# Kernel optimization log

Hardware: AMD Instinct MI355X
Metric: run time of the kernel (lower is better)

The kernel has to match this reference:

```python
import jax, jax.numpy as jnp
import numpy as np

SEQ, BATCH = 256, 8
N_NODES = SEQ * BATCH
VOCAB, D_MODEL, H, D_K, D_FF, N_LAYERS, MAX_POS = 259, 256, 8, 32, 1024, 2, 128


def setup_inputs() -> dict:
    key = jax.random.key(0)
    ks = jax.random.split(key, 16)
    # structured causal edge list per sequence (dst attends to src <= dst, incl. self)
    tri_dst, tri_src = np.tril_indices(SEQ)
    offs = (np.arange(BATCH) * SEQ)[:, None]
    edge_src = jnp.asarray((tri_src[None, :] + offs).ravel(), dtype=jnp.int64)
    edge_dst = jnp.asarray((tri_dst[None, :] + offs).ravel(), dtype=jnp.int64)
    positions = jnp.tile(jnp.arange(SEQ, dtype=jnp.int64), BATCH)
    tokens = jax.random.randint(ks[0], (N_NODES,), 0, VOCAB, dtype=jnp.int64)
    s = 0.02
    p = lambda k, shp: jax.random.normal(k, shp, dtype=jnp.float32) * s
    return {
        "tokens": tokens, "positions": positions,
        "edge_src": edge_src, "edge_dst": edge_dst,
        "coord_emb": p(ks[1], (3, D_MODEL)),
        "pos_emb": p(ks[2], (MAX_POS, D_MODEL)),
        "value_emb": p(ks[3], (VOCAB, D_MODEL)),
        "ln1_scale": jnp.ones((N_LAYERS, D_MODEL)), "ln1_bias": jnp.zeros((N_LAYERS, D_MODEL)),
        "Wqkv": p(ks[4], (N_LAYERS, D_MODEL, 3 * D_MODEL)),
        "Wo": p(ks[5], (N_LAYERS, D_MODEL, D_MODEL)),
        "ln2_scale": jnp.ones((N_LAYERS, D_MODEL)), "ln2_bias": jnp.zeros((N_LAYERS, D_MODEL)),
        "W1": p(ks[6], (N_LAYERS, D_MODEL, D_FF)), "b1": jnp.zeros((N_LAYERS, D_FF)),
        "W2": p(ks[7], (N_LAYERS, D_FF, D_MODEL)), "b2": jnp.zeros((N_LAYERS, D_MODEL)),
        "lnf_scale": jnp.ones((D_MODEL,)), "lnf_bias": jnp.zeros((D_MODEL,)),
        "Wg": p(ks[8], (D_MODEL, VOCAB)), "bg": jnp.zeros((VOCAB,)),
    }


def _ln(x, scale, bias, eps=1e-5):
    mu = jnp.mean(x, axis=-1, keepdims=True)
    var = jnp.var(x, axis=-1, keepdims=True)
    return (x - mu) * jax.lax.rsqrt(var + eps) * scale + bias


def _graph_attention(x, src, dst, Wqkv, Wo, ln_s, ln_b):
    n = x.shape[0]
    xn = _ln(x, ln_s, ln_b)
    qkv = (xn @ Wqkv).reshape(n, 3, H, D_K)
    q, k, v = qkv[:, 0], qkv[:, 1], qkv[:, 2]  # [n, H, D_K] each
    # u_dot_v('k','q','score') per edge, scaled
    score = jnp.einsum("ehd,ehd->eh", k[src], q[dst]) / jnp.sqrt(jnp.float32(D_K))
    # edge_softmax over incoming edges of each dst node
    smax = jax.ops.segment_max(score, dst, num_segments=n)      # [n, H]
    ex = jnp.exp(score - smax[dst])                              # [E, H]
    denom = jax.ops.segment_sum(ex, dst, num_segments=n)        # [n, H]
    alpha = ex / denom[dst]
    # u_mul_e('v','softmax_score') + sum reduce -> z on dst nodes
    z = jax.ops.segment_sum(alpha[:, :, None] * v[src], dst, num_segments=n)  # [n, H, D_K]
    return x + z.reshape(n, D_MODEL) @ Wo


def reference(tokens, positions, edge_src, edge_dst, coord_emb, pos_emb, value_emb,
              ln1_scale, ln1_bias, Wqkv, Wo, ln2_scale, ln2_bias, W1, b1, W2, b2,
              lnf_scale, lnf_bias, Wg, bg):
    x = coord_emb[positions % 3] + pos_emb[positions // 3] + value_emb[tokens]
    for i in range(Wqkv.shape[0]):
        x = _graph_attention(x, edge_src, edge_dst, Wqkv[i], Wo[i], ln1_scale[i], ln1_bias[i])
        h = _ln(x, ln2_scale[i], ln2_bias[i])
        x = x + jax.nn.relu(h @ W1[i] + b1[i]) @ W2[i] + b2[i]
    out = _ln(x, lnf_scale, lnf_bias) @ Wg + bg
    return jax.nn.log_softmax(out, axis=-1)
```

## Files before the change

kernel.cpp:

```cpp
#include <hip/hip_runtime.h>
#include <hip/hip_bf16.h>

typedef __hip_bfloat16 bf16;
typedef unsigned short ushort_t;
typedef unsigned int uint_t;
typedef __attribute__((ext_vector_type(8))) short short8;
typedef __attribute__((ext_vector_type(4))) float floatx4;

#define D_MODEL 256
#define SEQ     256
#define BATCH   8
#define NN      2048
#define NHEAD   8
#define DK      32
#define DFF     1024
#define VOCAB   259
#define NLAYER  2

#define WQKVT_OFF 0
#define WOT_OFF   393216
#define W1T_OFF   524288
#define W2T_OFF   1048576
#define WGT_OFF   1572864
#define WT_TOTAL  1639168
#define LNP_TOTAL 2560
#define BP_TOTAL  2819

__device__ __forceinline__ ushort_t f2bs(float f) {
    bf16 h = __float2bfloat16(f);
    ushort_t u; __builtin_memcpy(&u, &h, 2); return u;
}
template<bool BF>
__device__ __forceinline__ float ldw(const void* p, int i) {
    if (BF) return __bfloat162float(((const bf16*)p)[i]);
    return ((const float*)p)[i];
}
template<bool BF>
__device__ __forceinline__ ushort_t ldb(const void* p, size_t i) {
    if (BF) return ((const ushort_t*)p)[i];
    return f2bs(((const float*)p)[i]);
}
template<bool I64>
__device__ __forceinline__ int ldi(const void* p, int i) {
    if (I64) return (int)(((const long long*)p)[i]);
    return ((const int*)p)[i];
}
__device__ __forceinline__ float wred_sum(float v) {
    #pragma unroll
    for (int m = 32; m > 0; m >>= 1) v += __shfl_xor(v, m, 64);
    return v;
}
__device__ __forceinline__ float wred_max(float v) {
    #pragma unroll
    for (int m = 32; m > 0; m >>= 1) v = fmaxf(v, __shfl_xor(v, m, 64));
    return v;
}
__device__ __forceinline__ bool detBF(const void* ln1s) {
    return *(const uint_t*)ln1s == 0x3F803F80u;
}
__device__ __forceinline__ bool detI64(const void* pos) {
    const int* p32 = (const int*)pos;
    return p32[1] == 0 && p32[2] == 1;
}

template<bool BF>
__device__ void ttile(const void* src, size_t srcOff, int K, int N, int tk, int tn,
                      ushort_t* dst, ushort_t (*tile)[72]) {
    int t = threadIdx.x;
    if ((N & 63) == 0) {
        #pragma unroll
        for (int pass = 0; pass < 2; ++pass) {
            int e = pass * 256 + t;
            int kl = e >> 3, ng = e & 7;
            size_t sbase = srcOff + (size_t)(tk*64 + kl) * N + tn*64 + ng*8;
            ushort_t v[8];
            if (BF) {
                *reinterpret_cast<uint4*>(v) =
                    *reinterpret_cast<const uint4*>((const ushort_t*)src + sbase);
            } else {
                float4 a = *reinterpret_cast<const float4*>((const float*)src + sbase);
                float4 b = *reinterpret_cast<const float4*>((const float*)src + sbase + 4);
                v[0]=f2bs(a.x); v[1]=f2bs(a.y); v[2]=f2bs(a.z); v[3]=f2bs(a.w);
                v[4]=f2bs(b.x); v[5]=f2bs(b.y); v[6]=f2bs(b.z); v[7]=f2bs(b.w);
            }
            *reinterpret_cast<uint4*>(&tile[kl][ng*8]) = *reinterpret_cast<const uint4*>(v);
        }
        __syncthreads();
        #pragma unroll
        for (int pass = 0; pass < 2; ++pass) {
            int e = pass * 256 + t;
            int nl = e >> 3, kg = e & 7;
            int n = tn * 64 + nl;
            ushort_t v[8];
            #pragma unroll
            for (int j = 0; j < 8; ++j) v[j] = tile[kg*8 + j][nl];
            *reinterpret_cast<uint4*>(dst + (size_t)n * K + tk*64 + kg*8) =
                *reinterpret_cast<const uint4*>(v);
        }
    } else {
        #pragma unroll
        for (int pass = 0; pass < 16; ++pass) {
            int e = pass * 256 + t;
            int kl = e >> 6, nl = e & 63;
            int n = tn * 64 + nl;
            tile[kl][nl] = (n < N) ? ldb<BF>(src, srcOff + (size_t)(tk*64 + kl) * N + n)
                                   : (ushort_t)0;
        }
        __syncthreads();
        #pragma unroll
        for (int pass = 0; pass < 16; ++pass) {
            int e = pass * 256 + t;
            int nl = e >> 6, kl = e & 63;
            int n = tn * 64 + nl;
            if (n < N) dst[(size_t)n * K + tk*64 + kl] = tile[kl][nl];
        }
    }
}

template<bool BF, bool I64>
__device__ void embedln16(const void* tok, const void* pos,
        const void* ce, const void* pe, const void* ve,
        const void* ln1s, const void* ln1b, int rowBase,
        float* x, ushort_t* xn) {
    int lane = threadIdx.x & 63, wave = threadIdx.x >> 6;
    #pragma unroll
    for (int i = 0; i < 4; ++i) {
        int n = rowBase + wave * 4 + i;
        int p  = ldi<I64>(pos, n);
        int tk = ldi<I64>(tok, n);
        int c0 = lane * 4;
        float v[4];
        #pragma unroll
        for (int j = 0; j < 4; ++j)
            v[j] = ldw<BF>(ce, (p % 3) * 256 + c0 + j)
                 + ldw<BF>(pe, (p / 3) * 256 + c0 + j)
                 + ldw<BF>(ve, tk * 256 + c0 + j);
        float s  = wred_sum(v[0] + v[1] + v[2] + v[3]);
        float s2 = wred_sum(v[0]*v[0] + v[1]*v[1] + v[2]*v[2] + v[3]*v[3]);
        float mu = s * (1.f/256.f);
        float var = s2 * (1.f/256.f) - mu * mu;
        float rstd = rsqrtf(var + 1e-5f);
        *reinterpret_cast<float4*>(&x[(size_t)n*256 + c0]) =
            make_float4(v[0], v[1], v[2], v[3]);
        ushort4 o;
        o.x = f2bs((v[0]-mu)*rstd*ldw<BF>(ln1s, c0+0) + ldw<BF>(ln1b, c0+0));
        o.y = f2bs((v[1]-mu)*rstd*ldw<BF>(ln1s, c0+1) + ldw<BF>(ln1b, c0+1));
        o.z = f2bs((v[2]-mu)*rstd*ldw<BF>(ln1s, c0+2) + ldw<BF>(ln1b, c0+2));
        o.w = f2bs((v[3]-mu)*rstd*ldw<BF>(ln1s, c0+3) + ldw<BF>(ln1b, c0+3));
        *reinterpret_cast<ushort4*>(&xn[(size_t)n*256 + c0]) = o;
    }
}

template<bool BF, bool I64>
__device__ void prep_body(const void* tok, const void* pos,
        const void* ce, const void* pe, const void* ve,
        const void* Wqkv, const void* Wo, const void* W1, const void* W2, const void* Wg,
        const void* ln1s, const void* ln1b, const void* ln2s, const void* ln2b,
        const void* lnfs, const void* lnfb,
        const void* b1, const void* b2, const void* bg,
        ushort_t* WT, float* lnP, float* bP, float* x, ushort_t* xn,
        ushort_t (*tile)[72]) {
    int blk = blockIdx.x;
    if (blk < 404) {
        const void* src; int K, N, tk, tn; size_t dstOff, srcOff;
        if (blk < 96)       { int L = blk/48, lo = blk%48; src=Wqkv; K=256; N=768;
                              srcOff=(size_t)L*196608; dstOff=WQKVT_OFF+(size_t)L*196608;
                              tk=lo/12; tn=lo%12; }
        else if (blk < 128) { int b2=blk-96, L=b2/16, lo=b2%16; src=Wo; K=256; N=256;
                              srcOff=(size_t)L*65536; dstOff=WOT_OFF+(size_t)L*65536;
                              tk=lo/4; tn=lo%4; }
        else if (blk < 256) { int b2=blk-128, L=b2/64, lo=b2%64; src=W1; K=256; N=1024;
                              srcOff=(size_t)L*262144; dstOff=W1T_OFF+(size_t)L*262144;
                              tk=lo/16; tn=lo%16; }
        else if (blk < 384) { int b2=blk-256, L=b2/64, lo=b2%64; src=W2; K=1024; N=256;
                              srcOff=(size_t)L*262144; dstOff=W2T_OFF+(size_t)L*262144;
                              tk=lo/4; tn=lo%4; }
        else                { int lo=blk-384; src=Wg; K=256; N=259;
                              srcOff=0; dstOff=WGT_OFF; tk=lo/5; tn=lo%5; }
        ttile<BF>(src, srcOff, K, N, tk, tn, WT + dstOff, tile);
    } else if (blk < 426) {
        int gid = (blk - 404) * 256 + threadIdx.x;
        if (gid < LNP_TOTAL) {
            float v;
            if      (gid < 512)  v = ldw<BF>(ln1s, gid);
            else if (gid < 1024) v = ldw<BF>(ln1b, gid - 512);
            else if (gid < 1536) v = ldw<BF>(ln2s, gid - 1024);
            else if (gid < 2048) v = ldw<BF>(ln2b, gid - 1536);
            else if (gid < 2304) v = ldw<BF>(lnfs, gid - 2048);
            else                 v = ldw<BF>(lnfb, gid - 2304);
            lnP[gid] = v;
        } else if (gid < LNP_TOTAL + BP_TOTAL) {
            int g = gid - LNP_TOTAL;
            float v;
            if      (g < 2048) v = ldw<BF>(b1, g);
            else if (g < 2560) v = ldw<BF>(b2, g - 2048);
            else               v = ldw<BF>(bg, g - 2560);
            bP[g] = v;
        }
    } else {
        embedln16<BF, I64>(tok, pos, ce, pe, ve, ln1s, ln1b, (blk - 426) * 16, x, xn);
    }
}

__global__ void __launch_bounds__(256) prep_k(const void* tok, const void* pos,
        const void* ce, const void* pe, const void* ve,
        const void* Wqkv, const void* Wo, const void* W1, const void* W2, const void* Wg,
        const void* ln1s, const void* ln1b, const void* ln2s, const void* ln2b,
        const void* lnfs, const void* lnfb,
        const void* b1, const void* b2, const void* bg,
        ushort_t* WT, float* lnP, float* bP, float* x, ushort_t* xn) {
    __shared__ ushort_t tile[64][72];
    bool BF = detBF(ln1s), I64 = detI64(pos);
    if (BF) { if (I64) prep_body<true,true >(tok,pos,ce,pe,ve,Wqkv,Wo,W1,W2,Wg,ln1s,ln1b,ln2s,ln2b,lnfs,lnfb,b1,b2,bg,WT,lnP,bP,x,xn,tile);
              else     prep_body<true,false>(tok,pos,ce,pe,ve,Wqkv,Wo,W1,W2,Wg,ln1s,ln1b,ln2s,ln2b,lnfs,lnfb,b1,b2,bg,WT,lnP,bP,x,xn,tile); }
    else    { if (I64) prep_body<false,true >(tok,pos,ce,pe,ve,Wqkv,Wo,W1,W2,Wg,ln1s,ln1b,ln2s,ln2b,lnfs,lnfb,b1,b2,bg,WT,lnP,bP,x,xn,tile);
              else     prep_body<false,false>(tok,pos,ce,pe,ve,Wqkv,Wo,W1,W2,Wg,ln1s,ln1b,ln2s,ln2b,lnfs,lnfb,b1,b2,bg,WT,lnP,bP,x,xn,tile); }
}

union AttnSH {
    struct {
        ushort_t Ks[SEQ][40];
        ushort_t Qs[64][40];
    } a;
    ushort_t Ps[64][264];
};
__global__ void __launch_bounds__(256) attn_k(const ushort_t* __restrict__ qkvB,
                                              ushort_t* __restrict__ zB,
                                              float* __restrict__ yZ) {
    __shared__ AttnSH u;
    __shared__ ushort_t Vt[32][264];
    int t = threadIdx.x;
    {
        float4 z4 = make_float4(0.f, 0.f, 0.f, 0.f);
        float4* yp = reinterpret_cast<float4*>(yZ + (size_t)blockIdx.x * 2048);
        yp[t]       = z4;
        yp[t + 256] = z4;
    }
    int lane = t & 63, wave = t >> 6;
    int quad = lane >> 4, l16 = lane & 15;
    int tile = blockIdx.x & 3, bh = blockIdx.x >> 2;
    int b = bh >> 3, h = bh & 7;
    int base = b * SEQ;
    int dstBase = tile * 64;
    int tileEnd = (tile + 1) * 64;

    int nV = tileEnd * 4;
    for (int i = t; i < nV; i += 256) {
        int src = i >> 2, g = i & 3;
        const ushort_t* rp = qkvB + (size_t)(base + src) * 768 + h * 32 + g * 8;
        uint4 kv = *reinterpret_cast<const uint4*>(rp + 256);
        *reinterpret_cast<uint4*>(&u.a.Ks[src][g * 8]) = kv;
        uint4 vv = *reinterpret_cast<const uint4*>(rp + 512);
        const ushort_t* vs = (const ushort_t*)&vv;
        #pragma unroll
        for (int j = 0; j < 8; ++j) Vt[g * 8 + j][src] = vs[j];
    }
    {
        int r = t >> 2, g = t & 3;
        uint4 qv = *reinterpret_cast<const uint4*>(
            qkvB + (size_t)(base + dstBase + r) * 768 + h * 32 + g * 8);
        *reinterpret_cast<uint4*>(&u.a.Qs[r][g * 8]) = qv;
    }
    __syncthreads();

    const float scale = 0.17677669529663687f;
    int stLim = tile * 4 + wave;
    int stCnt = stLim + 1;
    short8 qf = *reinterpret_cast<const short8*>(&u.a.Qs[wave * 16 + l16][quad * 8]);
    floatx4 accs[16];
    #pragma unroll
    for (int st = 0; st < 16; ++st) {
        if (st <= stLim) {
            short8 kf = *reinterpret_cast<const short8*>(&u.a.Ks[st * 16 + l16][quad * 8]);
            accs[st] = __builtin_amdgcn_mfma_f32_16x16x32_bf16(qf, kf, (floatx4){0.f,0.f,0.f,0.f}, 0, 0, 0);
        }
    }
    float mrow[4] = {-3e38f, -3e38f, -3e38f, -3e38f};
    #pragma unroll
    for (int st = 0; st < 16; ++st) {
        if (st <= stLim) {
            int srcg = st * 16 + l16;
            #pragma unroll
            for (int r = 0; r < 4; ++r) {
                int dstg = dstBase + wave * 16 + quad * 4 + r;
                float sv = (srcg <= dstg) ? accs[st][r] * scale : -3e38f;
                accs[st][r] = sv;
                mrow[r] = fmaxf(mrow[r], sv);
            }
        }
    }
    #pragma unroll
    for (int mk = 1; mk < 16; mk <<= 1)
        #pragma unroll
        for (int r = 0; r < 4; ++r) mrow[r] = fmaxf(mrow[r], __shfl_xor(mrow[r], mk, 64));
    float lrow[4] = {0.f, 0.f, 0.f, 0.f};
    #pragma unroll
    for (int st = 0; st < 16; ++st) {
        if (st <= stLim) {
            #pragma unroll
            for (int r = 0; r < 4; ++r) {
                float p = __expf(accs[st][r] - mrow[r]);
                accs[st][r] = p;
                lrow[r] += p;
            }
        }
    }
    #pragma unroll
    for (int mk = 1; mk < 16; mk <<= 1)
        #pragma unroll
        for (int r = 0; r < 4; ++r) lrow[r] += __shfl_xor(lrow[r], mk, 64);
    __syncthreads();

    #pragma unroll
    for (int st = 0; st < 16; ++st) {
        if (st <= stLim) {
            #pragma unroll
            for (int r = 0; r < 4; ++r)
                u.Ps[wave * 16 + quad * 4 + r][st * 16 + l16] = f2bs(accs[st][r]);
        }
    }
    if (stCnt & 1) {
        #pragma unroll
        for (int r = 0; r < 4; ++r)
            u.Ps[wave * 16 + quad * 4 + r][stCnt * 16 + l16] = 0;
    }
    __syncthreads();

    int ktCnt = (stCnt + 1) >> 1;
    floatx4 acco[2];
    acco[0] = (floatx4){0.f,0.f,0.f,0.f};
    acco[1] = (floatx4){0.f,0.f,0.f,0.f};
    #pragma unroll
    for (int kt = 0; kt < 8; ++kt) {
        if (kt < ktCnt) {
            short8 pf = *reinterpret_cast<const short8*>(&u.Ps[wave * 16 + l16][kt * 32 + quad * 8]);
            #pragma unroll
            for (int dn = 0; dn < 2; ++dn) {
                short8 vf = *reinterpret_cast<const short8*>(&Vt[dn * 16 + l16][kt * 32 + quad * 8]);
                acco[dn] = __builtin_amdgcn_mfma_f32_16x16x32_bf16(pf, vf, acco[dn], 0, 0, 0);
            }
        }
    }
    #pragma unroll
    for (int dn = 0; dn < 2; ++dn)
        #pragma unroll
        for (int r = 0; r < 4; ++r)
            zB[(size_t)(base + dstBase + wave * 16 + quad * 4 + r) * 256
               + h * 32 + dn * 16 + l16] = f2bs(acco[dn][r] / lrow[r]);
}

__global__ void __launch_bounds__(256) gemm_k(const ushort_t* __restrict__ A, int K,
        const ushort_t* __restrict__ BT, const float* __restrict__ bias,
        ushort_t* __restrict__ C, int ldc, int relu) {
    int t = threadIdx.x;
    int lane = t & 63, wave = t >> 6;
    int quad = lane >> 4, l16 = lane & 15;
    int wm = (wave >> 1) * 32, wn = (wave & 1) * 32;
    int rowBase = blockIdx.x * 64, colBase = blockIdx.y * 64;
    floatx4 acc[2][2];
    #pragma unroll
    for (int a = 0; a < 2; ++a)
        #pragma unroll
        for (int b = 0; b < 2; ++b) acc[a][b] = (floatx4){0.f,0.f,0.f,0.f};
    const ushort_t* a0 = A + (size_t)(rowBase + wm + l16) * K + quad * 8;
    const ushort_t* a1 = a0 + (size_t)16 * K;
    const ushort_t* b0 = BT + (size_t)(colBase + wn + l16) * K + quad * 8;
    const ushort_t* b1 = b0 + (size_t)16 * K;
    #pragma unroll 8
    for (int k0 = 0; k0 < K; k0 += 32) {
        short8 af0 = *reinterpret_cast<const short8*>(a0 + k0);
        short8 af1 = *reinterpret_cast<const short8*>(a1 + k0);
        short8 bf0 = *reinterpret_cast<const short8*>(b0 + k0);
        short8 bf1 = *reinterpret_cast<const short8*>(b1 + k0);
        acc[0][0] = __builtin_amdgcn_mfma_f32_16x16x32_bf16(af0, bf0, acc[0][0], 0,0,0);
        acc[0][1] = __builtin_amdgcn_mfma_f32_16x16x32_bf16(af0, bf1, acc[0][1], 0,0,0);
        acc[1][0] = __builtin_amdgcn_mfma_f32_16x16x32_bf16(af1, bf0, acc[1][0], 0,0,0);
        acc[1][1] = __builtin_amdgcn_mfma_f32_16x16x32_bf16(af1, bf1, acc[1][1], 0,0,0);
    }
    #pragma unroll
    for (int nt = 0; nt < 2; ++nt) {
        int col = colBase + wn + nt*16 + l16;
        float bb = bias ? bias[col] : 0.f;
        #pragma unroll
        for (int mt = 0; mt < 2; ++mt)
            #pragma unroll
            for (int r = 0; r < 4; ++r) {
                int row = rowBase + wm + mt*16 + quad*4 + r;
                float v = acc[mt][nt][r] + bb;
                if (relu) v = fmaxf(v, 0.f);
                C[(size_t)row * ldc + col] = f2bs(v);
            }
    }
}

__global__ void __launch_bounds__(256) tail_k(
        const ushort_t* __restrict__ zB, const ushort_t* __restrict__ WoT,
        const float* __restrict__ xIn,
        const float* __restrict__ ls2, const float* __restrict__ lb2,
        const ushort_t* __restrict__ W1T, const float* __restrict__ b1P,
        const ushort_t* __restrict__ W2T, const float* __restrict__ b2P,
        float* __restrict__ yAcc) {
    __shared__ float    xrowS[32][256];
    __shared__ ushort_t xnA[32][264];
    ushort_t (*hmidS)[264] = reinterpret_cast<ushort_t (*)[264]>(&xrowS[0][0]);
    int t = threadIdx.x, lane = t & 63, wave = t >> 6;
    int quad = lane >> 4, l16 = lane & 15;
    int rowBase = blockIdx.x * 32, cg = blockIdx.y;
    float vpre[2][4][4];

    {
        floatx4 acc[2][4];
        #pragma unroll
        for (int mt = 0; mt < 2; ++mt)
            #pragma unroll
            for (int nt = 0; nt < 4; ++nt) acc[mt][nt] = (floatx4){0.f,0.f,0.f,0.f};
        const ushort_t* a0 = zB + (size_t)(rowBase + l16) * 256 + quad * 8;
        const ushort_t* a1 = a0 + (size_t)16 * 256;
        #pragma unroll
        for (int k0 = 0; k0 < 256; k0 += 32) {
            short8 af0 = *reinterpret_cast<const short8*>(a0 + k0);
            short8 af1 = *reinterpret_cast<const short8*>(a1 + k0);
            #pragma unroll
            for (int nt = 0; nt < 4; ++nt) {
                short8 bv = *reinterpret_cast<const short8*>(
                    WoT + (size_t)(wave*64 + nt*16 + l16) * 256 + k0 + quad * 8);
                acc[0][nt] = __builtin_amdgcn_mfma_f32_16x16x32_bf16(af0, bv, acc[0][nt], 0,0,0);
                acc[1][nt] = __builtin_amdgcn_mfma_f32_16x16x32_bf16(af1, bv, acc[1][nt], 0,0,0);
            }
        }
        #pragma unroll
        for (int nt = 0; nt < 4; ++nt) {
            int col = wave*64 + nt*16 + l16;
            #pragma unroll
            for (int mt = 0; mt < 2; ++mt)
                #pragma unroll
                for (int r = 0; r < 4; ++r) {
                    int row = mt*16 + quad*4 + r;
                    float v = acc[mt][nt][r] + xIn[(size_t)(rowBase + row) * 256 + col];
                    vpre[mt][nt][r] = v;
                    xrowS[row][col] = v;
                }
        }
    }
    __syncthreads();
    #pragma unroll
    for (int i = 0; i < 8; ++i) {
        int row = wave*8 + i, c0 = lane * 4;
        float4 vv = *reinterpret_cast<const float4*>(&xrowS[row][c0]);
        float s  = wred_sum(vv.x + vv.y + vv.z + vv.w);
        float s2 = wred_sum(vv.x*vv.x + vv.y*vv.y + vv.z*vv.z + vv.w*vv.w);
        float mu = s * (1.f/256.f);
        float var = s2 * (1.f/256.f) - mu*mu;
        float rstd = rsqrtf(var + 1e-5f);
        ushort4 o;
        o.x = f2bs((vv.x-mu)*rstd*ls2[c0+0] + lb2[c0+0]);
        o.y = f2bs((vv.y-mu)*rstd*ls2[c0+1] + lb2[c0+1]);
        o.z = f2bs((vv.z-mu)*rstd*ls2[c0+2] + lb2[c0+2]);
        o.w = f2bs((vv.w-mu)*rstd*ls2[c0+3] + lb2[c0+3]);
        *reinterpret_cast<ushort4*>(&xnA[row][c0]) = o;
    }
    __syncthreads();

    {
        floatx4 acc[2][4];
        #pragma unroll
        for (int mt = 0; mt < 2; ++mt)
            #pragma unroll
            for (int nt = 0; nt < 4; ++nt) acc[mt][nt] = (floatx4){0.f,0.f,0.f,0.f};
        const ushort_t* a0 = &xnA[l16][quad * 8];
        const ushort_t* a1 = &xnA[16 + l16][quad * 8];
        #pragma unroll
        for (int k0 = 0; k0 < 256; k0 += 32) {
            short8 af0 = *reinterpret_cast<const short8*>(a0 + k0);
            short8 af1 = *reinterpret_cast<const short8*>(a1 + k0);
            #pragma unroll
            for (int nt = 0; nt < 4; ++nt) {
                short8 bv = *reinterpret_cast<const short8*>(
                    W1T + (size_t)(cg*256 + wave*64 + nt*16 + l16) * 256 + k0 + quad * 8);
                acc[0][nt] = __builtin_amdgcn_mfma_f32_16x16x32_bf16(af0, bv, acc[0][nt], 0,0,0);
                acc[1][nt] = __builtin_amdgcn_mfma_f32_16x16x32_bf16(af1, bv, acc[1][nt], 0,0,0);
            }
        }
        __syncthreads();
        #pragma unroll
        for (int nt = 0; nt < 4; ++nt) {
            int lcol = wave*64 + nt*16 + l16;
            float bb = b1P[cg*256 + lcol];
            #pragma unroll
            for (int mt = 0; mt < 2; ++mt)
                #pragma unroll
                for (int r = 0; r < 4; ++r) {
                    int row = mt*16 + quad*4 + r;
                    hmidS[row][lcol] = f2bs(fmaxf(acc[mt][nt][r] + bb, 0.f));
                }
        }
    }
    __syncthreads();

    {
        floatx4 acc[2][4];
        #pragma unroll
        for (int mt = 0; mt < 2; ++mt)
            #pragma unroll
            for (int nt = 0; nt < 4; ++nt) acc[mt][nt] = (floatx4){0.f,0.f,0.f,0.f};
        const ushort_t* a0 = &hmidS[l16][quad * 8];
        const ushort_t* a1 = &hmidS[16 + l16][quad * 8];
        #pragma unroll
        for (int k0 = 0; k0 < 256; k0 += 32) {
            short8 af0 = *reinterpret_cast<const short8*>(a0 + k0);
            short8 af1 = *reinterpret_cast<const short8*>(a1 + k0);
            #pragma unroll
            for (int nt = 0; nt < 4; ++nt) {
                short8 bv = *reinterpret_cast<const short8*>(
                    W2T + (size_t)(wave*64 + nt*16 + l16) * 1024 + cg*256 + k0 + quad * 8);
                acc[0][nt] = __builtin_amdgcn_mfma_f32_16x16x32_bf16(af0, bv, acc[0][nt], 0,0,0);
                acc[1][nt] = __builtin_amdgcn_mfma_f32_16x16x32_bf16(af1, bv, acc[1][nt], 0,0,0);
            }
        }
        #pragma unroll
        for (int nt = 0; nt < 4; ++nt) {
            int col = wave*64 + nt*16 + l16;
            float bb = (cg == 0) ? b2P[col] : 0.f;
            #pragma unroll
            for (int mt = 0; mt < 2; ++mt)
                #pragma unroll
                for (int r = 0; r < 4; ++r) {
                    int row = mt*16 + quad*4 + r;
                    float add = acc[mt][nt][r];
                    if (cg == 0) add += vpre[mt][nt][r] + bb;
                    atomicAdd(&yAcc[(size_t)(rowBase + row) * 256 + col], add);
                }
        }
    }
}

__global__ void __launch_bounds__(256) lnqkv_k(
        const float* __restrict__ yIn,
        const float* __restrict__ ls, const float* __restrict__ lb,
        const ushort_t* __restrict__ WqkvT, ushort_t* __restrict__ qkvB) {
    __shared__ ushort_t xnA[64][264];
    int t = threadIdx.x, lane = t & 63, wave = t >> 6;
    int quad = lane >> 4, l16 = lane & 15;
    int rowBase = blockIdx.x * 64, colBase = blockIdx.y * 64;
    #pragma unroll
    for (int i = 0; i < 16; ++i) {
        int row = wave*16 + i, c0 = lane * 4;
        float4 vv = *reinterpret_cast<const float4*>(yIn + (size_t)(rowBase + row) * 256 + c0);
        float s  = wred_sum(vv.x + vv.y + vv.z + vv.w);
        float s2 = wred_sum(vv.x*vv.x + vv.y*vv.y + vv.z*vv.z + vv.w*vv.w);
        float mu = s * (1.f/256.f);
        float var = s2 * (1.f/256.f) - mu*mu;
        float rstd = rsqrtf(var + 1e-5f);
        ushort4 o;
        o.x = f2bs((vv.x-mu)*rstd*ls[c0+0] + lb[c0+0]);
        o.y = f2bs((vv.y-mu)*rstd*ls[c0+1] + lb[c0+1]);
        o.z = f2bs((vv.z-mu)*rstd*ls[c0+2] + lb[c0+2]);
        o.w = f2bs((vv.w-mu)*rstd*ls[c0+3] + lb[c0+3]);
        *reinterpret_cast<ushort4*>(&xnA[row][c0]) = o;
    }
    __syncthreads();
    int wm = (wave >> 1) * 32, wn = (wave & 1) * 32;
    floatx4 acc[2][2];
    #pragma unroll
    for (int a = 0; a < 2; ++a)
        #pragma unroll
        for (int b = 0; b < 2; ++b) acc[a][b] = (floatx4){0.f,0.f,0.f,0.f};
    const ushort_t* a0 = &xnA[wm + l16][quad * 8];
    const ushort_t* a1 = &xnA[wm + 16 + l16][quad * 8];
    #pragma unroll
    for (int k0 = 0; k0 < 256; k0 += 32) {
        short8 af0 = *reinterpret_cast<const short8*>(a0 + k0);
        short8 af1 = *reinterpret_cast<const short8*>(a1 + k0);
        #pragma unroll
        for (int nt = 0; nt < 2; ++nt) {
            short8 bv = *reinterpret_cast<const short8*>(
                WqkvT + (size_t)(colBase + wn + nt*16 + l16) * 256 + k0 + quad * 8);
            acc[0][nt] = __builtin_amdgcn_mfma_f32_16x16x32_bf16(af0, bv, acc[0][nt], 0,0,0);
            acc[1][nt] = __builtin_amdgcn_mfma_f32_16x16x32_bf16(af1, bv, acc[1][nt], 0,0,0);
        }
    }
    #pragma unroll
    for (int nt = 0; nt < 2; ++nt) {
        int col = colBase + wn + nt*16 + l16;
        #pragma unroll
        for (int mt = 0; mt < 2; ++mt)
            #pragma unroll
            for (int r = 0; r < 4; ++r) {
                int row = wm + mt*16 + quad*4 + r;
                qkvB[(size_t)(rowBase + row) * 768 + col] = f2bs(acc[mt][nt][r]);
            }
    }
}

__global__ void __launch_bounds__(256) lnlg_k(
        const float* __restrict__ yIn,
        const float* __restrict__ lnfsP, const float* __restrict__ lnfbP,
        const ushort_t* __restrict__ WgT, const float* __restrict__ bgP,
        const void* __restrict__ ln1sRaw, void* __restrict__ outp) {
    __shared__ float    xrow[16][256];
    __shared__ ushort_t xnA[16][264];
    __shared__ float    Lg[16][273];
    int t = threadIdx.x, lane = t & 63, wave = t >> 6;
    int quad = lane >> 4, l16 = lane & 15;
    int rowBase = blockIdx.x * 16;
    #pragma unroll
    for (int i = 0; i < 4; ++i) {
        int idx = i * 256 + t;
        int row = idx >> 6, c4 = (idx & 63) * 4;
        *reinterpret_cast<float4*>(&xrow[row][c4]) =
            *reinterpret_cast<const float4*>(yIn + (size_t)(rowBase + row) * 256 + c4);
    }
    __syncthreads();
    #pragma unroll
    for (int i = 0; i < 4; ++i) {
        int row = wave*4 + i, c0 = lane * 4;
        float4 vv = *reinterpret_cast<const float4*>(&xrow[row][c0]);
        float s  = wred_sum(vv.x + vv.y + vv.z + vv.w);
        float s2 = wred_sum(vv.x*vv.x + vv.y*vv.y + vv.z*vv.z + vv.w*vv.w);
        float mu = s * (1.f/256.f);
        float var = s2 * (1.f/256.f) - mu*mu;
        float rstd = rsqrtf(var + 1e-5f);
        ushort4 o;
        o.x = f2bs((vv.x-mu)*rstd*lnfsP[c0+0] + lnfbP[c0+0]);
        o.y = f2bs((vv.y-mu)*rstd*lnfsP[c0+1] + lnfbP[c0+1]);
        o.z = f2bs((vv.z-mu)*rstd*lnfsP[c0+2] + lnfbP[c0+2]);
        o.w = f2bs((vv.w-mu)*rstd*lnfsP[c0+3] + lnfbP[c0+3]);
        *reinterpret_cast<ushort4*>(&xnA[row][c0]) = o;
    }
    __syncthreads();
    const ushort_t* a0 = &xnA[l16][quad * 8];
    int cb = wave * 64;
    {
        floatx4 acc[4];
        #pragma unroll
        for (int nt = 0; nt < 4; ++nt) acc[nt] = (floatx4){0.f,0.f,0.f,0.f};
        #pragma unroll
        for (int kc = 0; kc < 8; ++kc) {
            short8 af = *reinterpret_cast<const short8*>(a0 + kc * 32);
            #pragma unroll
            for (int nt = 0; nt < 4; ++nt) {
                short8 bv = *reinterpret_cast<const short8*>(
                    WgT + (size_t)(cb + nt*16 + l16) * 256 + kc*32 + quad*8);
                acc[nt] = __builtin_amdgcn_mfma_f32_16x16x32_bf16(af, bv, acc[nt], 0,0,0);
            }
        }
        #pragma unroll
        for (int nt = 0; nt < 4; ++nt) {
            int col = cb + nt*16 + l16;
            float bb = bgP[col];
            #pragma unroll
            for (int r = 0; r < 4; ++r)
                Lg[quad*4 + r][col] = acc[nt][r] + bb;
        }
    }
    if (wave == 0) {
        floatx4 acc = (floatx4){0.f,0.f,0.f,0.f};
        int n = 256 + l16;
        int nc = (n < VOCAB) ? n : 0;
        const ushort_t* b0 = WgT + (size_t)nc * 256 + quad * 8;
        #pragma unroll
        for (int kc = 0; kc < 8; ++kc) {
            short8 af = *reinterpret_cast<const short8*>(a0 + kc * 32);
            short8 bv = *reinterpret_cast<const short8*>(b0 + kc * 32);
            acc = __builtin_amdgcn_mfma_f32_16x16x32_bf16(af, bv, acc, 0,0,0);
        }
        #pragma unroll
        for (int r = 0; r < 4; ++r)
            Lg[quad*4 + r][256 + l16] = (n < VOCAB) ? (acc[r] + bgP[n]) : -1e30f;
    }
    __syncthreads();
    int outBF = detBF(ln1sRaw) ? 1 : 0;
    #pragma unroll
    for (int i = 0; i < 4; ++i) {
        int row = wave*4 + i;
        float v0 = Lg[row][lane],     v1 = Lg[row][lane+64];
        float v2 = Lg[row][lane+128], v3 = Lg[row][lane+192];
        float v4 = (lane < 16) ? Lg[row][256+lane] : -1e30f;
        float m = wred_max(fmaxf(fmaxf(fmaxf(v0,v1), fmaxf(v2,v3)), v4));
        float se = __expf(v0-m) + __expf(v1-m) + __expf(v2-m) + __expf(v3-m)
                 + ((lane < 16) ? __expf(v4-m) : 0.f);
        se = wred_sum(se);
        float lse = m + logf(se);
        size_t nbase = (size_t)(rowBase + row) * VOCAB;
        if (outBF) {
            ushort_t* o = (ushort_t*)outp + nbase;
            o[lane]     = f2bs(v0 - lse);
            o[lane+64]  = f2bs(v1 - lse);
            o[lane+128] = f2bs(v2 - lse);
            o[lane+192] = f2bs(v3 - lse);
            if (lane < 3) o[256+lane] = f2bs(v4 - lse);
        } else {
            float* o = (float*)outp + nbase;
            o[lane]     = v0 - lse;
            o[lane+64]  = v1 - lse;
            o[lane+128] = v2 - lse;
            o[lane+192] = v3 - lse;
            if (lane < 3) o[256+lane] = v4 - lse;
        }
    }
}

extern "C" void kernel_launch(void* const* d_in, const int* in_sizes, int n_in,
                              void* d_out, int out_size, void* d_ws, size_t ws_size,
                              hipStream_t stream) {
    const void* tok  = d_in[0];
    const void* pos  = d_in[1];
    const void* ce   = d_in[4];
    const void* pe   = d_in[5];
    const void* ve   = d_in[6];
    const void* ln1s = d_in[7];
    const void* ln1b = d_in[8];
    const void* Wqkv = d_in[9];
    const void* Wo   = d_in[10];
    const void* ln2s = d_in[11];
    const void* ln2b = d_in[12];
    const void* W1   = d_in[13];
    const void* b1   = d_in[14];
    const void* W2   = d_in[15];
    const void* b2   = d_in[16];
    const void* lnfs = d_in[17];
    const void* lnfb = d_in[18];
    const void* Wg   = d_in[19];
    const void* bg   = d_in[20];

    char* base = (char*)d_ws;
    float*    lnP   = (float*)base;
    float*    bP    = (float*)(base + 10240);
    float*    xA    = (float*)(base + 22528);
    ushort_t* xn    = (ushort_t*)(base + 2119680);
    ushort_t* zB    = (ushort_t*)(base + 3168256);
    ushort_t* WT    = (ushort_t*)(base + 8411136);
    ushort_t* qkvB  = (ushort_t*)(base + 11689472);
    float*    xB    = (float*)(base + 14835200);
    float*    xC    = (float*)(base + 16932352);

    prep_k<<<554, 256, 0, stream>>>(tok, pos, ce, pe, ve,
        Wqkv, Wo, W1, W2, Wg, ln1s, ln1b, ln2s, ln2b, lnfs, lnfb,
        b1, b2, bg, WT, lnP, bP, xA, xn);

    gemm_k<<<dim3(32, 12), 256, 0, stream>>>(xn, 256,
        WT + WQKVT_OFF, nullptr, qkvB, 768, 0);

    attn_k<<<256, 256, 0, stream>>>(qkvB, zB, xB);

    tail_k<<<dim3(64, 4), 256, 0, stream>>>(zB, WT + WOT_OFF, xA,
        lnP + 1024, lnP + 1536, WT + W1T_OFF, bP, WT + W2T_OFF, bP + 2048, xB);

    lnqkv_k<<<dim3(32, 12), 256, 0, stream>>>(xB, lnP + 256, lnP + 768,
        WT + WQKVT_OFF + 196608, qkvB);

    attn_k<<<256, 256, 0, stream>>>(qkvB, zB, xC);

    tail_k<<<dim3(64, 4), 256, 0, stream>>>(zB, WT + WOT_OFF + 65536, xB,
        lnP + 1024 + 256, lnP + 1536 + 256, WT + W1T_OFF + 262144, bP + 1024,
        WT + W2T_OFF + 262144, bP + 2048 + 256, xC);

    lnlg_k<<<128, 256, 0, stream>>>(xC, lnP + 2048, lnP + 2304,
        WT + WGT_OFF, bP + 2560, ln1s, d_out);
}
```

Baseline: 204.3 us.

## Defer non-layer-0 weight transposes into the QKV GEMM launch

The prep kernel now transposes only the layer-0 Wqkv weights, plus the LN/bias copies and the embedding+LN. The remaining weight transposes (layer-1 Wqkv, Wo, W1, W2, Wg) run as extra blocks inside a new combined kernel alongside the first QKV GEMM. This shrinks the critical path before the first GEMM and overlaps transpose work with it. The embedding loads are also vectorised to 4-wide. The combined kernel has a larger, heterogeneous grid in which GEMM and transpose blocks compete for CUs.

After: 202.8 us. About the same (-0.7%).

```diff
diff --git a/kernel.cpp b/kernel.cpp
--- a/kernel.cpp
+++ b/kernel.cpp
@@ -30,6 +30,9 @@
     bf16 h = __float2bfloat16(f);
     ushort_t u; __builtin_memcpy(&u, &h, 2); return u;
 }
+__device__ __forceinline__ float bs2f(ushort_t u) {
+    return __uint_as_float((uint_t)u << 16);
+}
 template<bool BF>
 __device__ __forceinline__ float ldw(const void* p, int i) {
     if (BF) return __bfloat162float(((const bf16*)p)[i]);
@@ -44,6 +47,16 @@
 __device__ __forceinline__ int ldi(const void* p, int i) {
     if (I64) return (int)(((const long long*)p)[i]);
     return ((const int*)p)[i];
+}
+template<bool BF>
+__device__ __forceinline__ void ldw4(const void* p, int i, float* o) {
+    if (BF) {
+        ushort4 u = *reinterpret_cast<const ushort4*>((const ushort_t*)p + i);
+        o[0] = bs2f(u.x); o[1] = bs2f(u.y); o[2] = bs2f(u.z); o[3] = bs2f(u.w);
+    } else {
+        float4 f = *reinterpret_cast<const float4*>((const float*)p + i);
+        o[0] = f.x; o[1] = f.y; o[2] = f.z; o[3] = f.w;
+    }
 }
 __device__ __forceinline__ float wred_sum(float v) {
     #pragma unroll
@@ -129,12 +142,12 @@
         int p  = ldi<I64>(pos, n);
         int tk = ldi<I64>(tok, n);
         int c0 = lane * 4;
-        float v[4];
-        #pragma unroll
-        for (int j = 0; j < 4; ++j)
-            v[j] = ldw<BF>(ce, (p % 3) * 256 + c0 + j)
-                 + ldw<BF>(pe, (p / 3) * 256 + c0 + j)
-                 + ldw<BF>(ve, tk * 256 + c0 + j);
+        float vc[4], vp[4], vv4[4], v[4];
+        ldw4<BF>(ce, (p % 3) * 256 + c0, vc);
+        ldw4<BF>(pe, (p / 3) * 256 + c0, vp);
+        ldw4<BF>(ve, tk * 256 + c0, vv4);
+        #pragma unroll
+        for (int j = 0; j < 4; ++j) v[j] = vc[j] + vp[j] + vv4[j];
         float s  = wred_sum(v[0] + v[1] + v[2] + v[3]);
         float s2 = wred_sum(v[0]*v[0] + v[1]*v[1] + v[2]*v[2] + v[3]*v[3]);
         float mu = s * (1.f/256.f);
@@ -142,11 +155,14 @@
         float rstd = rsqrtf(var + 1e-5f);
         *reinterpret_cast<float4*>(&x[(size_t)n*256 + c0]) =
             make_float4(v[0], v[1], v[2], v[3]);
+        float ls4[4], lb4[4];
+        ldw4<BF>(ln1s, c0, ls4);
+        ldw4<BF>(ln1b, c0, lb4);
         ushort4 o;
-        o.x = f2bs((v[0]-mu)*rstd*ldw<BF>(ln1s, c0+0) + ldw<BF>(ln1b, c0+0));
-        o.y = f2bs((v[1]-mu)*rstd*ldw<BF>(ln1s, c0+1) + ldw<BF>(ln1b, c0+1));
-        o.z = f2bs((v[2]-mu)*rstd*ldw<BF>(ln1s, c0+2) + ldw<BF>(ln1b, c0+2));
-        o.w = f2bs((v[3]-mu)*rstd*ldw<BF>(ln1s, c0+3) + ldw<BF>(ln1b, c0+3));
+        o.x = f2bs((v[0]-mu)*rstd*ls4[0] + lb4[0]);
+        o.y = f2bs((v[1]-mu)*rstd*ls4[1] + lb4[1]);
+        o.z = f2bs((v[2]-mu)*rstd*ls4[2] + lb4[2]);
+        o.w = f2bs((v[3]-mu)*rstd*ls4[3] + lb4[3]);
         *reinterpret_cast<ushort4*>(&xn[(size_t)n*256 + c0]) = o;
     }
 }
@@ -154,32 +170,18 @@
 template<bool BF, bool I64>
 __device__ void prep_body(const void* tok, const void* pos,
         const void* ce, const void* pe, const void* ve,
-        const void* Wqkv, const void* Wo, const void* W1, const void* W2, const void* Wg,
+        const void* Wqkv,
         const void* ln1s, const void* ln1b, const void* ln2s, const void* ln2b,
         const void* lnfs, const void* lnfb,
         const void* b1, const void* b2, const void* bg,
         ushort_t* WT, float* lnP, float* bP, float* x, ushort_t* xn,
         ushort_t (*tile)[72]) {
     int blk = blockIdx.x;
-    if (blk < 404) {
-        const void* src; int K, N, tk, tn; size_t dstOff, srcOff;
-        if (blk < 96)       { int L = blk/48, lo = blk%48; src=Wqkv; K=256; N=768;
-                              srcOff=(size_t)L*196608; dstOff=WQKVT_OFF+(size_t)L*196608;
-                              tk=lo/12; tn=lo%12; }
-        else if (blk < 128) { int b2=blk-96, L=b2/16, lo=b2%16; src=Wo; K=256; N=256;
-                              srcOff=(size_t)L*65536; dstOff=WOT_OFF+(size_t)L*65536;
-                              tk=lo/4; tn=lo%4; }
-        else if (blk < 256) { int b2=blk-128, L=b2/64, lo=b2%64; src=W1; K=256; N=1024;
-                              srcOff=(size_t)L*262144; dstOff=W1T_OFF+(size_t)L*262144;
-                              tk=lo/16; tn=lo%16; }
-        else if (blk < 384) { int b2=blk-256, L=b2/64, lo=b2%64; src=W2; K=1024; N=256;
-                              srcOff=(size_t)L*262144; dstOff=W2T_OFF+(size_t)L*262144;
-                              tk=lo/4; tn=lo%4; }
-        else                { int lo=blk-384; src=Wg; K=256; N=259;
-                              srcOff=0; dstOff=WGT_OFF; tk=lo/5; tn=lo%5; }
-        ttile<BF>(src, srcOff, K, N, tk, tn, WT + dstOff, tile);
-    } else if (blk < 426) {
-        int gid = (blk - 404) * 256 + threadIdx.x;
+    if (blk < 48) {
+        int lo = blk;
+        ttile<BF>(Wqkv, 0, 256, 768, lo/12, lo%12, WT + WQKVT_OFF, tile);
+    } else if (blk < 70) {
+        int gid = (blk - 48) * 256 + threadIdx.x;
         if (gid < LNP_TOTAL) {
             float v;
             if      (gid < 512)  v = ldw<BF>(ln1s, gid);
@@ -198,23 +200,96 @@
             bP[g] = v;
         }
     } else {
-        embedln16<BF, I64>(tok, pos, ce, pe, ve, ln1s, ln1b, (blk - 426) * 16, x, xn);
+        embedln16<BF, I64>(tok, pos, ce, pe, ve, ln1s, ln1b, (blk - 70) * 16, x, xn);
     }
 }
 
 __global__ void __launch_bounds__(256) prep_k(const void* tok, const void* pos,
         const void* ce, const void* pe, const void* ve,
-        const void* Wqkv, const void* Wo, const void* W1, const void* W2, const void* Wg,
+        const void* Wqkv,
         const void* ln1s, const void* ln1b, const void* ln2s, const void* ln2b,
         const void* lnfs, const void* lnfb,
         const void* b1, const void* b2, const void* bg,
         ushort_t* WT, float* lnP, float* bP, float* x, ushort_t* xn) {
     __shared__ ushort_t tile[64][72];
     bool BF = detBF(ln1s), I64 = detI64(pos);
-    if (BF) { if (I64) prep_body<true,true >(tok,pos,ce,pe,ve,Wqkv,Wo,W1,W2,Wg,ln1s,ln1b,ln2s,ln2b,lnfs,lnfb,b1,b2,bg,WT,lnP,bP,x,xn,tile);
-              else     prep_body<true,false>(tok,pos,ce,pe,ve,Wqkv,Wo,W1,W2,Wg,ln1s,ln1b,ln2s,ln2b,lnfs,lnfb,b1,b2,bg,WT,lnP,bP,x,xn,tile); }
-    else    { if (I64) prep_body<false,true >(tok,pos,ce,pe,ve,Wqkv,Wo,W1,W2,Wg,ln1s,ln1b,ln2s,ln2b,lnfs,lnfb,b1,b2,bg,WT,lnP,bP,x,xn,tile);
-              else     prep_body<false,false>(tok,pos,ce,pe,ve,Wqkv,Wo,W1,W2,Wg,ln1s,ln1b,ln2s,ln2b,lnfs,lnfb,b1,b2,bg,WT,lnP,bP,x,xn,tile); }
+    if (BF) { if (I64) prep_body<true,true >(tok,pos,ce,pe,ve,Wqkv,ln1s,ln1b,ln2s,ln2b,lnfs,lnfb,b1,b2,bg,WT,lnP,bP,x,xn,tile);
+              else     prep_body<true,false>(tok,pos,ce,pe,ve,Wqkv,ln1s,ln1b,ln2s,ln2b,lnfs,lnfb,b1,b2,bg,WT,lnP,bP,x,xn,tile); }
+    else    { if (I64) prep_body<false,true >(tok,pos,ce,pe,ve,Wqkv,ln1s,ln1b,ln2s,ln2b,lnfs,lnfb,b1,b2,bg,WT,lnP,bP,x,xn,tile);
+              else     prep_body<false,false>(tok,pos,ce,pe,ve,Wqkv,ln1s,ln1b,ln2s,ln2b,lnfs,lnfb,b1,b2,bg,WT,lnP,bP,x,xn,tile); }
+}
+
+template<bool BF>
+__device__ void qkvt_body(const ushort_t* __restrict__ xn,
+        const ushort_t* __restrict__ WqkvT0, ushort_t* __restrict__ qkvB,
+        const void* Wqkv, const void* Wo, const void* W1, const void* W2, const void* Wg,
+        ushort_t* WT, ushort_t (*tile)[72]) {
+    int bid = blockIdx.x;
+    if (bid < 384) {
+        int t = threadIdx.x;
+        int lane = t & 63, wave = t >> 6;
+        int quad = lane >> 4, l16 = lane & 15;
+        int wm = (wave >> 1) * 32, wn = (wave & 1) * 32;
+        int rowBase = (bid & 31) * 64, colBase = (bid >> 5) * 64;
+        floatx4 acc[2][2];
+        #pragma unroll
+        for (int a = 0; a < 2; ++a)
+            #pragma unroll
+            for (int b = 0; b < 2; ++b) acc[a][b] = (floatx4){0.f,0.f,0.f,0.f};
+        const ushort_t* a0 = xn + (size_t)(rowBase + wm + l16) * 256 + quad * 8;
+        const ushort_t* a1 = a0 + (size_t)16 * 256;
+        const ushort_t* b0 = WqkvT0 + (size_t)(colBase + wn + l16) * 256 + quad * 8;
+        const ushort_t* b1 = b0 + (size_t)16 * 256;
+        #pragma unroll 8
+        for (int k0 = 0; k0 < 256; k0 += 32) {
+            short8 af0 = *reinterpret_cast<const short8*>(a0 + k0);
+            short8 af1 = *reinterpret_cast<const short8*>(a1 + k0);
+            short8 bf0 = *reinterpret_cast<const short8*>(b0 + k0);
+            short8 bf1 = *reinterpret_cast<const short8*>(b1 + k0);
+            acc[0][0] = __builtin_amdgcn_mfma_f32_16x16x32_bf16(af0, bf0, acc[0][0], 0,0,0);
+            acc[0][1] = __builtin_amdgcn_mfma_f32_16x16x32_bf16(af0, bf1, acc[0][1], 0,0,0);
+            acc[1][0] = __builtin_amdgcn_mfma_f32_16x16x32_bf16(af1, bf0, acc[1][0], 0,0,0);
+            acc[1][1] = __builtin_amdgcn_mfma_f32_16x16x32_bf16(af1, bf1, acc[1][1], 0,0,0);
+        }
+        #pragma unroll
+        for (int nt = 0; nt < 2; ++nt) {
+            int col = colBase + wn + nt*16 + l16;
+            #pragma unroll
+            for (int mt = 0; mt < 2; ++mt)
+                #pragma unroll
+                for (int r = 0; r < 4; ++r) {
+                    int row = rowBase + wm + mt*16 + quad*4 + r;
+                    qkvB[(size_t)row * 768 + col] = f2bs(acc[mt][nt][r]);
+                }
+        }
+    } else {
+        int task = bid - 384;
+        const void* src; int K, N, tk, tn; size_t dstOff, srcOff;
+        if (task < 48)       { int lo = task; src=Wqkv; K=256; N=768;
+                               srcOff=196608; dstOff=WQKVT_OFF+196608;
+                               tk=lo/12; tn=lo%12; }
+        else if (task < 80)  { int t2=task-48, L=t2/16, lo=t2%16; src=Wo; K=256; N=256;
+                               srcOff=(size_t)L*65536; dstOff=WOT_OFF+(size_t)L*65536;
+                               tk=lo/4; tn=lo%4; }
+        else if (task < 208) { int t2=task-80, L=t2/64, lo=t2%64; src=W1; K=256; N=1024;
+                               srcOff=(size_t)L*262144; dstOff=W1T_OFF+(size_t)L*262144;
+                               tk=lo/16; tn=lo%16; }
+        else if (task < 336) { int t2=task-208, L=t2/64, lo=t2%64; src=W2; K=1024; N=256;
+                               srcOff=(size_t)L*262144; dstOff=W2T_OFF+(size_t)L*262144;
+                               tk=lo/4; tn=lo%4; }
+        else                 { int lo=task-336; src=Wg; K=256; N=259;
+                               srcOff=0; dstOff=WGT_OFF; tk=lo/5; tn=lo%5; }
+        ttile<BF>(src, srcOff, K, N, tk, tn, WT + dstOff, tile);
+    }
+}
+
+__global__ void __launch_bounds__(256) qkvt_k(const ushort_t* __restrict__ xn,
+        const ushort_t* __restrict__ WqkvT0, ushort_t* __restrict__ qkvB,
+        const void* Wqkv, const void* Wo, const void* W1, const void* W2, const void* Wg,
+        ushort_t* WT, const void* ln1s) {
+    __shared__ ushort_t tile[64][72];
+    if (detBF(ln1s)) qkvt_body<true >(xn, WqkvT0, qkvB, Wqkv, Wo, W1, W2, Wg, WT, tile);
+    else             qkvt_body<false>(xn, WqkvT0, qkvB, Wqkv, Wo, W1, W2, Wg, WT, tile);
 }
 
 union AttnSH {
@@ -347,50 +422,6 @@
         for (int r = 0; r < 4; ++r)
             zB[(size_t)(base + dstBase + wave * 16 + quad * 4 + r) * 256
                + h * 32 + dn * 16 + l16] = f2bs(acco[dn][r] / lrow[r]);
-}
-
-__global__ void __launch_bounds__(256) gemm_k(const ushort_t* __restrict__ A, int K,
-        const ushort_t* __restrict__ BT, const float* __restrict__ bias,
-        ushort_t* __restrict__ C, int ldc, int relu) {
-    int t = threadIdx.x;
-    int lane = t & 63, wave = t >> 6;
-    int quad = lane >> 4, l16 = lane & 15;
-    int wm = (wave >> 1) * 32, wn = (wave & 1) * 32;
-    int rowBase = blockIdx.x * 64, colBase = blockIdx.y * 64;
-    floatx4 acc[2][2];
-    #pragma unroll
-    for (int a = 0; a < 2; ++a)
-        #pragma unroll
-        for (int b = 0; b < 2; ++b) acc[a][b] = (floatx4){0.f,0.f,0.f,0.f};
-    const ushort_t* a0 = A + (size_t)(rowBase + wm + l16) * K + quad * 8;
-    const ushort_t* a1 = a0 + (size_t)16 * K;
-    const ushort_t* b0 = BT + (size_t)(colBase + wn + l16) * K + quad * 8;
-    const ushort_t* b1 = b0 + (size_t)16 * K;
-    #pragma unroll 8
-    for (int k0 = 0; k0 < K; k0 += 32) {
-        short8 af0 = *reinterpret_cast<const short8*>(a0 + k0);
-        short8 af1 = *reinterpret_cast<const short8*>(a1 + k0);
-        short8 bf0 = *reinterpret_cast<const short8*>(b0 + k0);
-        short8 bf1 = *reinterpret_cast<const short8*>(b1 + k0);
-        acc[0][0] = __builtin_amdgcn_mfma_f32_16x16x32_bf16(af0, bf0, acc[0][0], 0,0,0);
-        acc[0][1] = __builtin_amdgcn_mfma_f32_16x16x32_bf16(af0, bf1, acc[0][1], 0,0,0);
-        acc[1][0] = __builtin_amdgcn_mfma_f32_16x16x32_bf16(af1, bf0, acc[1][0], 0,0,0);
-        acc[1][1] = __builtin_amdgcn_mfma_f32_16x16x32_bf16(af1, bf1, acc[1][1], 0,0,0);
-    }
-    #pragma unroll
-    for (int nt = 0; nt < 2; ++nt) {
-        int col = colBase + wn + nt*16 + l16;
-        float bb = bias ? bias[col] : 0.f;
-        #pragma unroll
-        for (int mt = 0; mt < 2; ++mt)
-            #pragma unroll
-            for (int r = 0; r < 4; ++r) {
-                int row = rowBase + wm + mt*16 + quad*4 + r;
-                float v = acc[mt][nt][r] + bb;
-                if (relu) v = fmaxf(v, 0.f);
-                C[(size_t)row * ldc + col] = f2bs(v);
-            }
-    }
 }
 
 __global__ void __launch_bounds__(256) tail_k(
@@ -734,12 +765,11 @@
     float*    xB    = (float*)(base + 14835200);
     float*    xC    = (float*)(base + 16932352);
 
-    prep_k<<<554, 256, 0, stream>>>(tok, pos, ce, pe, ve,
-        Wqkv, Wo, W1, W2, Wg, ln1s, ln1b, ln2s, ln2b, lnfs, lnfb,
-        b1, b2, bg, WT, lnP, bP, xA, xn);
-
-    gemm_k<<<dim3(32, 12), 256, 0, stream>>>(xn, 256,
-        WT + WQKVT_OFF, nullptr, qkvB, 768, 0);
+    prep_k<<<198, 256, 0, stream>>>(tok, pos, ce, pe, ve, Wqkv,
+        ln1s, ln1b, ln2s, ln2b, lnfs, lnfb, b1, b2, bg, WT, lnP, bP, xA, xn);
+
+    qkvt_k<<<740, 256, 0, stream>>>(xn, WT + WQKVT_OFF, qkvB,
+        Wqkv, Wo, W1, W2, Wg, WT, ln1s);
 
     attn_k<<<256, 256, 0, stream>>>(qkvB, zB, xB);
 
```
